# Kernel optimization log

Measured on AMD Instinct MI355X. Metric: run time of the kernel, lower is better.

Reference implementation:

```python
import jax, jax.numpy as jnp
import numpy as np

NHEAD = 16


def setup_inputs() -> dict:
    key = jax.random.key(0)
    ks = jax.random.split(key, 8)
    S, B, D = 2048, 2, 1024
    std = 1.0 / np.sqrt(D)
    src = jax.random.normal(ks[0], (S, B, D), dtype=jnp.float32)
    edge_bias_2d = jax.random.normal(ks[1], (S, S), dtype=jnp.float32)
    wq = jax.random.normal(ks[2], (D, D), dtype=jnp.float32) * std
    wk = jax.random.normal(ks[3], (D, D), dtype=jnp.float32) * std
    wv = jax.random.normal(ks[4], (D, D), dtype=jnp.float32) * std
    wo = jax.random.normal(ks[5], (D, D), dtype=jnp.float32) * std
    bq = jnp.zeros((D,), jnp.float32)
    bk = jnp.zeros((D,), jnp.float32)
    bv = jnp.zeros((D,), jnp.float32)
    bo = jnp.zeros((D,), jnp.float32)
    return {"src": src, "edge_bias_2d": edge_bias_2d, "wq": wq, "bq": bq,
            "wk": wk, "bk": bk, "wv": wv, "bv": bv, "wo": wo, "bo": bo}


def reference(src, edge_bias_2d, wq, bq, wk, bk, wv, bv, wo, bo):
    S, B, D = src.shape
    h = NHEAD
    hd = D // h
    scale = hd ** (-0.5)

    def heads(t):  # [S,B,D] -> [B,h,S,hd]
        return t.reshape(S, B, h, hd).transpose(1, 2, 0, 3)

    q = heads(src @ wq + bq)
    k = heads(src @ wk + bk)
    v = heads(src @ wv + bv)

    # [B,h,S,S]
    logits = jnp.einsum('bhsd,bhtd->bhst', q, k) * scale
    logits = logits + edge_bias_2d[None, None, :, :]
    attn = jax.nn.softmax(logits, axis=-1)
    # signed aggregation: sign(edge_bias) with 0 -> +1
    sign_gate = jnp.where(edge_bias_2d < 0, -1.0, 1.0).astype(attn.dtype)
    attn = attn * sign_gate[None, None, :, :]

    out = jnp.einsum('bhst,bhtd->bhsd', attn, v)  # [B,h,S,hd]
    out = out.transpose(2, 0, 1, 3).reshape(S, B, D)
    out = out @ wo + bo
    return out
```

## Files before the change

### kernel.cpp

```cpp
#include <hip/hip_runtime.h>
#include <stdint.h>

typedef unsigned short u16;
typedef unsigned int u32;

typedef __bf16 bf8 __attribute__((ext_vector_type(8)));
typedef bf8 bf8a __attribute__((may_alias));
typedef float f32x4 __attribute__((ext_vector_type(4)));
typedef uint2 uint2a __attribute__((may_alias));
typedef ushort4 ushort4a __attribute__((may_alias));
typedef float4 float4a __attribute__((may_alias));

#define MFMA_BF16(a, b, c) __builtin_amdgcn_mfma_f32_16x16x32_bf16((a), (b), (c), 0, 0, 0)

__device__ __forceinline__ u16 f2b(float x) {
  u32 u = __float_as_uint(x);
  return (u16)((u + 0x7fffu + ((u >> 16) & 1u)) >> 16);
}
__device__ __forceinline__ u32 pack2(float a, float b) {
  u32 ua = __float_as_uint(a), ub = __float_as_uint(b);
  return ((ua + 0x8000u) >> 16) | ((ub + 0x8000u) & 0xffff0000u);
}
__device__ __forceinline__ void async16(const u16* g, void* l) {
  __builtin_amdgcn_global_load_lds((const __attribute__((address_space(1))) u32*)g,
                                   (__attribute__((address_space(3))) u32*)l, 16, 0, 0);
}

__global__ __launch_bounds__(256) void convert_src(const float* __restrict__ src,
                                                   u16* __restrict__ dst) {
  const int i = blockIdx.x * 256 + threadIdx.x;
  float4 v = *(const float4a*)(src + i * 4);
  ushort4 o;
  o.x = f2b(v.x); o.y = f2b(v.y); o.z = f2b(v.z); o.w = f2b(v.w);
  *(ushort4a*)(dst + i * 4) = o;
}

__global__ __launch_bounds__(256) void prep_eb(const float* __restrict__ EB,
                                               u16* __restrict__ E2) {
  const int gid = blockIdx.x * 256 + threadIdx.x;
  const int s = gid >> 9;
  const int t = (gid & 511) * 4;
  const float4 v = *(const float4a*)(EB + s * 2048 + t);
  const float c2 = 1.44269504088896340736f;
  ushort4 o;
  o.x = f2b(__builtin_amdgcn_exp2f(v.x * c2)) | (u16)((__float_as_uint(v.x) >> 16) & 0x8000u);
  o.y = f2b(__builtin_amdgcn_exp2f(v.y * c2)) | (u16)((__float_as_uint(v.y) >> 16) & 0x8000u);
  o.z = f2b(__builtin_amdgcn_exp2f(v.z * c2)) | (u16)((__float_as_uint(v.z) >> 16) & 0x8000u);
  o.w = f2b(__builtin_amdgcn_exp2f(v.w * c2)) | (u16)((__float_as_uint(v.w) >> 16) & 0x8000u);
  const int ti = ((s >> 4) * 128 + (t >> 4)) * 256 + (s & 15) * 16 + (t & 15);
  *(ushort4a*)(E2 + ti) = o;
}

__global__ __launch_bounds__(256) void transpose4(
    const float* __restrict__ w0, const float* __restrict__ w1,
    const float* __restrict__ w2, const float* __restrict__ w3,
    u16* __restrict__ t0, u16* __restrict__ t1, u16* __restrict__ t2, u16* __restrict__ t3) {
  const int z = blockIdx.z;
  const float* W = z == 0 ? w0 : z == 1 ? w1 : z == 2 ? w2 : w3;
  u16* T = z == 0 ? t0 : z == 1 ? t1 : z == 2 ? t2 : t3;
  __shared__ __align__(8) u16 tile[64][68];
  const int tid = threadIdx.x;
  const int ty = tid >> 4, tx = tid & 15;
  const int kb = blockIdx.y * 64, nb = blockIdx.x * 64;
#pragma unroll
  for (int i = 0; i < 4; ++i) {
    int lk = ty + i * 16;
    float4 v = *(const float4a*)(W + (kb + lk) * 1024 + nb + tx * 4);
    ushort4 h;
    h.x = f2b(v.x); h.y = f2b(v.y); h.z = f2b(v.z); h.w = f2b(v.w);
    *(ushort4a*)&tile[lk][tx * 4] = h;
  }
  __syncthreads();
#pragma unroll
  for (int i = 0; i < 4; ++i) {
    int ln = ty + i * 16;
    ushort4 v;
    v.x = tile[tx * 4 + 0][ln];
    v.y = tile[tx * 4 + 1][ln];
    v.z = tile[tx * 4 + 2][ln];
    v.w = tile[tx * 4 + 3][ln];
    *(ushort4a*)(T + (nb + ln) * 1024 + kb + tx * 4) = v;
  }
}

__global__ __launch_bounds__(256) void gemm_bt(
    const u16* __restrict__ A,
    const u16* __restrict__ B0, const u16* __restrict__ B1, const u16* __restrict__ B2,
    const float* __restrict__ c0, const float* __restrict__ c1, const float* __restrict__ c2,
    u16* __restrict__ O0, u16* __restrict__ O1, u16* __restrict__ O2,
    float* __restrict__ Of, int plain) {
  __shared__ __align__(16) u16 sm[8192];
  u16* As = sm;
  u16* Bs = sm + 4096;
  const int tid = threadIdx.x, lane = tid & 63, w = tid >> 6;
  const int wm = w >> 1, wn = w & 1, quad = lane >> 4, l16 = lane & 15;
  const int z = blockIdx.z;
  const u16* Bt = z == 0 ? B0 : (z == 1 ? B1 : B2);
  const float* bi = z == 0 ? c0 : (z == 1 ? c1 : c2);
  u16* O = z == 0 ? O0 : (z == 1 ? O1 : O2);
  const int row0 = blockIdx.y * 128, col0 = blockIdx.x * 128;

  f32x4 acc[4][4];
#pragma unroll
  for (int i = 0; i < 4; ++i)
#pragma unroll
    for (int j = 0; j < 4; ++j) acc[i][j] = f32x4{0.f, 0.f, 0.f, 0.f};

  const int e0 = tid, e1 = tid + 256;
  const int r0 = e0 >> 2, cc0 = (e0 & 3) * 8;
  const int r1 = e1 >> 2, cc1 = (e1 & 3) * 8;
  const u32 lb0 = (u32)(w * 64) * 16;
  const u32 lb1 = (u32)(w * 64 + 256) * 16;

  for (int k0 = 0; k0 < 1024; k0 += 32) {
    __syncthreads();
    async16(A + (row0 + r0) * 1024 + k0 + cc0, (char*)As + lb0);
    async16(A + (row0 + r1) * 1024 + k0 + cc1, (char*)As + lb1);
    async16(Bt + (col0 + r0) * 1024 + k0 + cc0, (char*)Bs + lb0);
    async16(Bt + (col0 + r1) * 1024 + k0 + cc1, (char*)Bs + lb1);
    __syncthreads();
    bf8a af[4], bfr[4];
#pragma unroll
    for (int i = 0; i < 4; ++i) {
      af[i] = *(const bf8a*)(As + (wm * 64 + i * 16 + l16) * 32 + quad * 8);
      bfr[i] = *(const bf8a*)(Bs + (wn * 64 + i * 16 + l16) * 32 + quad * 8);
    }
#pragma unroll
    for (int mt = 0; mt < 4; ++mt)
#pragma unroll
      for (int nt = 0; nt < 4; ++nt) acc[mt][nt] = MFMA_BF16(af[mt], bfr[nt], acc[mt][nt]);
  }

#pragma unroll
  for (int nt = 0; nt < 4; ++nt) {
    const int col = col0 + wn * 64 + nt * 16 + l16;
    const float bcol = bi[col];
#pragma unroll
    for (int mt = 0; mt < 4; ++mt) {
#pragma unroll
      for (int r = 0; r < 4; ++r) {
        const int rm = row0 + wm * 64 + mt * 16 + quad * 4 + r;
        const float fv = acc[mt][nt][r] + bcol;
        if (plain) {
          Of[rm * 1024 + col] = fv;
        } else {
          const u16 hv = f2b(fv);
          const int s = rm >> 1, b_ = rm & 1, hh = col >> 6, e = col & 63;
          const int p = b_ * 16 + hh;
          if (z < 2) O[(p * 2048 + s) * 64 + e] = hv;
          else O[(p * 64 + e) * 2048 + s] = hv;
        }
      }
    }
  }
}

#define STAGE_K(Ksbuf, kt_)                                                         \
  {                                                                                 \
    _Pragma("unroll") for (int c = 0; c < 4; ++c) {                                 \
      const int row_ = c * 32 + w * 8 + r8;                                         \
      async16(Kp + ((kt_) * 128 + row_) * 64 + c16s * 8,                            \
              (char*)(Ksbuf) + (c * 4 + w) * 1024);                                 \
    }                                                                               \
  }

#define LOAD_E(eb, kt_)                                                             \
  {                                                                                 \
    const int tb16_ = (kt_) * 8 + w * 2;                                            \
    _Pragma("unroll") for (int st = 0; st < 4; ++st)                                \
      _Pragma("unroll") for (int tt = 0; tt < 2; ++tt)                              \
        eb[st][tt] = *(const uint2a*)(EBp + ((qt * 4 + st) * 128 + tb16_ + tt) * 256 \
                                      + l16 * 16 + quad * 4);                       \
  }

#define COMPUTE(Ksbuf, eb, kt_)                                                     \
  {                                                                                 \
    const int tb_ = (kt_) * 128 + w * 32;                                           \
    bf8a vf[4];            \
    _Pragma("unroll") for (int nt = 0; nt < 4; ++nt)                                \
      vf[nt] = *(const bf8a*)(Vp + (nt * 16 + l16) * 2048 + tb_ + quad * 8);        \
    bf8a kf[2][2];                                                                  \
    _Pragma("unroll") for (int tt = 0; tt < 2; ++tt) {                              \
      const int row_ = w * 32 + tt * 16 + l16;                 \
      _Pragma("unroll") for (int ks = 0; ks < 2; ++ks) {                            \
        const int cc_ = ((ks * 4 + quad) ^ (l16 & 7)) * 8;                          \
        kf[tt][ks] = *(const bf8a*)((Ksbuf) + row_ * 64 + cc_);                     \
      }                                                                             \
    }                                                                               \
    f32x4 sacc[4][2];                                                 \
    __builtin_amdgcn_s_setprio(1);                                                  \
    _Pragma("unroll") for (int tt = 0; tt < 2; ++tt)                                \
      _Pragma("unroll") for (int st = 0; st < 4; ++st) {                            \
        f32x4 t0_ = f32x4{0.f, 0.f, 0.f, 0.f};                                      \
        t0_ = MFMA_BF16(kf[tt][0], qf[st][0], t0_);                                 \
        sacc[st][tt] = MFMA_BF16(kf[tt][1], qf[st][1], t0_);                        \
      }                                                                             \
    __builtin_amdgcn_s_setprio(0);                                                  \
    _Pragma("unroll") for (int st = 0; st < 4; ++st) {                              \
      _Pragma("unroll") for (int tt = 0; tt < 2; ++tt) {                            \
        const uint2 e_ = eb[st][tt];                                                \
        const float g0 = __uint_as_float(e_.x << 16);                               \
        const float g1 = __uint_as_float(e_.x & 0xffff0000u);                       \
        const float g2 = __uint_as_float(e_.y << 16);                               \
        const float g3 = __uint_as_float(e_.y & 0xffff0000u);                       \
        const float p0 = __builtin_amdgcn_exp2f(sacc[st][tt][0] * c1) * g0;         \
        const float p1 = __builtin_amdgcn_exp2f(sacc[st][tt][1] * c1) * g1;         \
        const float p2 = __builtin_amdgcn_exp2f(sacc[st][tt][2] * c1) * g2;         \
        const float p3 = __builtin_amdgcn_exp2f(sacc[st][tt][3] * c1) * g3;         \
        lsum[st] += (__builtin_fabsf(p0) + __builtin_fabsf(p1)) +                   \
                    (__builtin_fabsf(p2) + __builtin_fabsf(p3));                    \
        uint2 v_;                                                                   \
        v_.x = pack2(p0, p1);                                                       \
        v_.y = pack2(p2, p3);                                                       \
        *(uint2a*)(Pw + st * 1152 + l16 * 72 + tt * 32 + quad * 8) = v_;            \
      }                                                                             \
    }                                                                               \
    _Pragma("unroll") for (int st = 0; st < 4; ++st) {                              \
      bf8a pf = *(const bf8a*)(Pw + st * 1152 + l16 * 72 + quad * 16);              \
      __builtin_amdgcn_s_setprio(1);                                                \
      _Pragma("unroll") for (int nt = 0; nt < 4; ++nt)                              \
        oacc[st][nt] = MFMA_BF16(vf[nt], pf, oacc[st][nt]);                         \
      __builtin_amdgcn_s_setprio(0);                                                \
    }                                                                               \
  }

__global__ __launch_bounds__(256, 2) void attn_fused(
    const u16* __restrict__ Qw, const u16* __restrict__ Kw, const u16* __restrict__ Vw,
    const u16* __restrict__ EBp, u16* __restrict__ Ao) {
  __shared__ __align__(16) char smem[51456];
  u16* const Ks0 = (u16*)smem;
  u16* const Ks1 = (u16*)(smem + 16384);
  const int tid = threadIdx.x, lane = tid & 63, w = tid >> 6;
  const int quad = lane >> 4, l16 = lane & 15;
  const int id = blockIdx.x;
  const int xcd = id & 7, idx = id >> 3;
  const int pair = xcd * 4 + (idx & 3);
  const int qt = idx >> 2;
  const int bb = pair >> 4, hh = pair & 15;
  const u16* Qp = Qw + pair * (2048 * 64);
  const u16* Kp = Kw + pair * (2048 * 64);
  const u16* Vp = Vw + pair * (64 * 2048);
  const int s0 = qt * 64;
  char* const Pw = smem + 32768 + w * 4608;

  bf8a qf[4][2];
#pragma unroll
  for (int st = 0; st < 4; ++st)
#pragma unroll
    for (int ks = 0; ks < 2; ++ks)
      qf[st][ks] = *(const bf8a*)(Qp + (s0 + st * 16 + l16) * 64 + ks * 32 + quad * 8);

  f32x4 oacc[4][4];
#pragma unroll
  for (int i = 0; i < 4; ++i)
#pragma unroll
    for (int j = 0; j < 4; ++j) oacc[i][j] = f32x4{0.f, 0.f, 0.f, 0.f};
  float lsum[4] = {0.f, 0.f, 0.f, 0.f};
  const float c1 = 0.125f * 1.44269504088896340736f;

  const int r8 = lane >> 3;
  const int c16s = (lane & 7) ^ r8;

  uint2 ebA[4][2], ebB[4][2];

  STAGE_K(Ks0, 0)
  LOAD_E(ebA, 0)
  __syncthreads();

  for (int kt = 0; kt < 16; kt += 2) {
    STAGE_K(Ks1, kt + 1)
    LOAD_E(ebB, kt + 1)
    COMPUTE(Ks0, ebA, kt)
    __syncthreads();
    if (kt < 14) {
      STAGE_K(Ks0, kt + 2)
      LOAD_E(ebA, kt + 2)
    }
    COMPUTE(Ks1, ebB, kt + 1)
    __syncthreads();
  }

  float* const Obuf = (float*)smem;
  float* const Lbuf = (float*)(smem + 51200);
#pragma unroll
  for (int st = 0; st < 4; ++st) {
    float ls = lsum[st];
    ls += __shfl_xor(ls, 16);
    ls += __shfl_xor(ls, 32);
    if (lane < 16) Lbuf[w * 16 + l16] = ls;
#pragma unroll
    for (int nt = 0; nt < 4; ++nt)
      *(float4a*)&Obuf[w * 1056 + l16 * 66 + nt * 16 + quad * 4] = (float4){
          oacc[st][nt][0], oacc[st][nt][1], oacc[st][nt][2], oacc[st][nt][3]};
    __syncthreads();
    {
      const int s_ = tid & 15, eg = (tid >> 4) * 4;
      float a0 = 0.f, a1 = 0.f, a2 = 0.f, a3 = 0.f;
#pragma unroll
      for (int wp = 0; wp < 4; ++wp) {
        const float4 x = *(const float4a*)&Obuf[wp * 1056 + s_ * 66 + eg];
        a0 += x.x; a1 += x.y; a2 += x.z; a3 += x.w;
      }
      const float lt = Lbuf[s_] + Lbuf[16 + s_] + Lbuf[32 + s_] + Lbuf[48 + s_];
      const float inv = 1.0f / lt;
      ushort4 o;
      o.x = f2b(a0 * inv); o.y = f2b(a1 * inv); o.z = f2b(a2 * inv); o.w = f2b(a3 * inv);
      *(ushort4a*)(Ao + ((s0 + st * 16 + s_) * 2 + bb) * 1024 + hh * 64 + eg) = o;
    }
    if (st < 3) __syncthreads();
  }
}

extern "C" void kernel_launch(void* const* d_in, const int* in_sizes, int n_in,
                              void* d_out, int out_size, void* d_ws, size_t ws_size,
                              hipStream_t stream) {
  const float* src = (const float*)d_in[0];
  const float* eb = (const float*)d_in[1];
  const float* wq = (const float*)d_in[2];
  const float* bq = (const float*)d_in[3];
  const float* wk = (const float*)d_in[4];
  const float* bk = (const float*)d_in[5];
  const float* wv = (const float*)d_in[6];
  const float* bv = (const float*)d_in[7];
  const float* wo = (const float*)d_in[8];
  const float* bo = (const float*)d_in[9];
  u16* ws = (u16*)d_ws;
  const size_t MM = 1024 * 1024;
  u16* wqT = ws;
  u16* wkT = ws + MM;
  u16* wvT = ws + 2 * MM;
  u16* woT = ws + 3 * MM;
  u16* srcB = ws + 4 * MM;
  u16* eb2 = ws + 4 * MM;
  u16* qW = ws + 8 * MM;
  u16* kW = ws + 12 * MM;
  u16* vW = ws + 16 * MM;
  u16* aO = ws + 20 * MM;
  float* out = (float*)d_out;

  convert_src<<<dim3(4096), 256, 0, stream>>>(src, srcB);
  transpose4<<<dim3(16, 16, 4), 256, 0, stream>>>(wq, wk, wv, wo, wqT, wkT, wvT, woT);
  gemm_bt<<<dim3(8, 32, 3), 256, 0, stream>>>(srcB, wqT, wkT, wvT, bq, bk, bv,
                                              qW, kW, vW, nullptr, 0);
  prep_eb<<<dim3(4096), 256, 0, stream>>>(eb, eb2);
  attn_fused<<<dim3(1024), 256, 0, stream>>>(qW, kW, vW, eb2, aO);
  gemm_bt<<<dim3(8, 32, 1), 256, 0, stream>>>(aO, woT, woT, woT, bo, bo, bo,
                                              nullptr, nullptr, nullptr, out, 1);
}
```

Before: 259.2 us.

## Fold softmax scale into Q projection, merge prep kernels, raise attention occupancy

Merges the source conversion and weight transpose into one launch. Folds the softmax scale and log2e factor into the Q projection epilogue so the attention kernel skips a multiply per score. Restructures the attention compute to process one 16-key sub-tile at a time, load the edge-bias tiles inside the compute step instead of double-buffering them in registers, and load V fragments later. Together these cut register pressure enough to request 3 blocks per SM instead of 2. It also switches P packing to the compiler's bf16 conversion. The cost is less latency hiding for the bias loads, and scaled Q is now rounded to bf16 after scaling, which slightly changes numerics.

```diff
diff --git a/kernel.cpp b/kernel.cpp
--- a/kernel.cpp
+++ b/kernel.cpp
@@ -17,22 +17,52 @@
   u32 u = __float_as_uint(x);
   return (u16)((u + 0x7fffu + ((u >> 16) & 1u)) >> 16);
 }
-__device__ __forceinline__ u32 pack2(float a, float b) {
-  u32 ua = __float_as_uint(a), ub = __float_as_uint(b);
-  return ((ua + 0x8000u) >> 16) | ((ub + 0x8000u) & 0xffff0000u);
-}
 __device__ __forceinline__ void async16(const u16* g, void* l) {
   __builtin_amdgcn_global_load_lds((const __attribute__((address_space(1))) u32*)g,
                                    (__attribute__((address_space(3))) u32*)l, 16, 0, 0);
 }
 
-__global__ __launch_bounds__(256) void convert_src(const float* __restrict__ src,
-                                                   u16* __restrict__ dst) {
-  const int i = blockIdx.x * 256 + threadIdx.x;
-  float4 v = *(const float4a*)(src + i * 4);
-  ushort4 o;
-  o.x = f2b(v.x); o.y = f2b(v.y); o.z = f2b(v.z); o.w = f2b(v.w);
-  *(ushort4a*)(dst + i * 4) = o;
+__global__ __launch_bounds__(256) void prep_inputs(
+    const float* __restrict__ src, u16* __restrict__ dst,
+    const float* __restrict__ w0, const float* __restrict__ w1,
+    const float* __restrict__ w2, const float* __restrict__ w3,
+    u16* __restrict__ t0, u16* __restrict__ t1, u16* __restrict__ t2, u16* __restrict__ t3) {
+  const int bid = blockIdx.x, tid = threadIdx.x;
+  if (bid < 4096) {
+    const int i = bid * 256 + tid;
+    float4 v = *(const float4a*)(src + i * 4);
+    ushort4 o;
+    o.x = f2b(v.x); o.y = f2b(v.y); o.z = f2b(v.z); o.w = f2b(v.w);
+    *(ushort4a*)(dst + i * 4) = o;
+    return;
+  }
+  const int b2 = bid - 4096;
+  const int z = b2 >> 8, xy = b2 & 255;
+  const int bx = xy & 15, by = xy >> 4;
+  const float* W = z == 0 ? w0 : z == 1 ? w1 : z == 2 ? w2 : w3;
+  u16* T = z == 0 ? t0 : z == 1 ? t1 : z == 2 ? t2 : t3;
+  __shared__ __align__(8) u16 tile[64][68];
+  const int ty = tid >> 4, tx = tid & 15;
+  const int kb = by * 64, nb = bx * 64;
+#pragma unroll
+  for (int i = 0; i < 4; ++i) {
+    int lk = ty + i * 16;
+    float4 v = *(const float4a*)(W + (kb + lk) * 1024 + nb + tx * 4);
+    ushort4 h;
+    h.x = f2b(v.x); h.y = f2b(v.y); h.z = f2b(v.z); h.w = f2b(v.w);
+    *(ushort4a*)&tile[lk][tx * 4] = h;
+  }
+  __syncthreads();
+#pragma unroll
+  for (int i = 0; i < 4; ++i) {
+    int ln = ty + i * 16;
+    ushort4 v;
+    v.x = tile[tx * 4 + 0][ln];
+    v.y = tile[tx * 4 + 1][ln];
+    v.z = tile[tx * 4 + 2][ln];
+    v.w = tile[tx * 4 + 3][ln];
+    *(ushort4a*)(T + (nb + ln) * 1024 + kb + tx * 4) = v;
+  }
 }
 
 __global__ __launch_bounds__(256) void prep_eb(const float* __restrict__ EB,
@@ -51,42 +81,11 @@
   *(ushort4a*)(E2 + ti) = o;
 }
 
-__global__ __launch_bounds__(256) void transpose4(
-    const float* __restrict__ w0, const float* __restrict__ w1,
-    const float* __restrict__ w2, const float* __restrict__ w3,
-    u16* __restrict__ t0, u16* __restrict__ t1, u16* __restrict__ t2, u16* __restrict__ t3) {
-  const int z = blockIdx.z;
-  const float* W = z == 0 ? w0 : z == 1 ? w1 : z == 2 ? w2 : w3;
-  u16* T = z == 0 ? t0 : z == 1 ? t1 : z == 2 ? t2 : t3;
-  __shared__ __align__(8) u16 tile[64][68];
-  const int tid = threadIdx.x;
-  const int ty = tid >> 4, tx = tid & 15;
-  const int kb = blockIdx.y * 64, nb = blockIdx.x * 64;
-#pragma unroll
-  for (int i = 0; i < 4; ++i) {
-    int lk = ty + i * 16;
-    float4 v = *(const float4a*)(W + (kb + lk) * 1024 + nb + tx * 4);
-    ushort4 h;
-    h.x = f2b(v.x); h.y = f2b(v.y); h.z = f2b(v.z); h.w = f2b(v.w);
-    *(ushort4a*)&tile[lk][tx * 4] = h;
-  }
-  __syncthreads();
-#pragma unroll
-  for (int i = 0; i < 4; ++i) {
-    int ln = ty + i * 16;
-    ushort4 v;
-    v.x = tile[tx * 4 + 0][ln];
-    v.y = tile[tx * 4 + 1][ln];
-    v.z = tile[tx * 4 + 2][ln];
-    v.w = tile[tx * 4 + 3][ln];
-    *(ushort4a*)(T + (nb + ln) * 1024 + kb + tx * 4) = v;
-  }
-}
-
 __global__ __launch_bounds__(256) void gemm_bt(
     const u16* __restrict__ A,
     const u16* __restrict__ B0, const u16* __restrict__ B1, const u16* __restrict__ B2,
     const float* __restrict__ c0, const float* __restrict__ c1, const float* __restrict__ c2,
+    float sc0, float sc1, float sc2,
     u16* __restrict__ O0, u16* __restrict__ O1, u16* __restrict__ O2,
     float* __restrict__ Of, int plain) {
   __shared__ __align__(16) u16 sm[8192];
@@ -97,6 +96,7 @@
   const int z = blockIdx.z;
   const u16* Bt = z == 0 ? B0 : (z == 1 ? B1 : B2);
   const float* bi = z == 0 ? c0 : (z == 1 ? c1 : c2);
+  const float sc = z == 0 ? sc0 : (z == 1 ? sc1 : sc2);
   u16* O = z == 0 ? O0 : (z == 1 ? O1 : O2);
   const int row0 = blockIdx.y * 128, col0 = blockIdx.x * 128;
 
@@ -140,7 +140,7 @@
 #pragma unroll
       for (int r = 0; r < 4; ++r) {
         const int rm = row0 + wm * 64 + mt * 16 + quad * 4 + r;
-        const float fv = acc[mt][nt][r] + bcol;
+        const float fv = (acc[mt][nt][r] + bcol) * sc;
         if (plain) {
           Of[rm * 1024 + col] = fv;
         } else {
@@ -164,57 +164,57 @@
     }                                                                               \
   }
 
-#define LOAD_E(eb, kt_)                                                             \
+#define COMPUTE(Ksbuf, kt_)                                                         \
   {                                                                                 \
     const int tb16_ = (kt_) * 8 + w * 2;                                            \
-    _Pragma("unroll") for (int st = 0; st < 4; ++st)                                \
-      _Pragma("unroll") for (int tt = 0; tt < 2; ++tt)                              \
-        eb[st][tt] = *(const uint2a*)(EBp + ((qt * 4 + st) * 128 + tb16_ + tt) * 256 \
-                                      + l16 * 16 + quad * 4);                       \
-  }
-
-#define COMPUTE(Ksbuf, eb, kt_)                                                     \
-  {                                                                                 \
-    const int tb_ = (kt_) * 128 + w * 32;                                           \
-    bf8a vf[4];            \
-    _Pragma("unroll") for (int nt = 0; nt < 4; ++nt)                                \
-      vf[nt] = *(const bf8a*)(Vp + (nt * 16 + l16) * 2048 + tb_ + quad * 8);        \
-    bf8a kf[2][2];                                                                  \
+    uint2 ebt[2][4];                          \
+    _Pragma("unroll") for (int tt = 0; tt < 2; ++tt)                                \
+      _Pragma("unroll") for (int st = 0; st < 4; ++st)                              \
+        ebt[tt][st] = *(const uint2a*)(EBp + ((qt * 4 + st) * 128 + tb16_ + tt) * 256 \
+                                       + l16 * 16 + quad * 4);                      \
     _Pragma("unroll") for (int tt = 0; tt < 2; ++tt) {                              \
-      const int row_ = w * 32 + tt * 16 + l16;                 \
-      _Pragma("unroll") for (int ks = 0; ks < 2; ++ks) {                            \
-        const int cc_ = ((ks * 4 + quad) ^ (l16 & 7)) * 8;                          \
-        kf[tt][ks] = *(const bf8a*)((Ksbuf) + row_ * 64 + cc_);                     \
+      bf8a kfa[2];                                                                  \
+      {                                                                             \
+        const int row_ = w * 32 + tt * 16 + l16;               \
+        _Pragma("unroll") for (int ks = 0; ks < 2; ++ks) {                          \
+          const int cc_ = ((ks * 4 + quad) ^ (l16 & 7)) * 8;                        \
+          kfa[ks] = *(const bf8a*)((Ksbuf) + row_ * 64 + cc_);                      \
+        }                                                                           \
       }                                                                             \
-    }                                                                               \
-    f32x4 sacc[4][2];                                                 \
-    __builtin_amdgcn_s_setprio(1);                                                  \
-    _Pragma("unroll") for (int tt = 0; tt < 2; ++tt)                                \
+      f32x4 sacc[4];                                                                \
+      __builtin_amdgcn_s_setprio(1);                                                \
       _Pragma("unroll") for (int st = 0; st < 4; ++st) {                            \
         f32x4 t0_ = f32x4{0.f, 0.f, 0.f, 0.f};                                      \
-        t0_ = MFMA_BF16(kf[tt][0], qf[st][0], t0_);                                 \
-        sacc[st][tt] = MFMA_BF16(kf[tt][1], qf[st][1], t0_);                        \
+        t0_ = MFMA_BF16(kfa[0], qf[st][0], t0_);                                    \
+        sacc[st] = MFMA_BF16(kfa[1], qf[st][1], t0_);                               \
       }                                                                             \
-    __builtin_amdgcn_s_setprio(0);                                                  \
-    _Pragma("unroll") for (int st = 0; st < 4; ++st) {                              \
-      _Pragma("unroll") for (int tt = 0; tt < 2; ++tt) {                            \
-        const uint2 e_ = eb[st][tt];                                                \
+      __builtin_amdgcn_s_setprio(0);                                                \
+      _Pragma("unroll") for (int st = 0; st < 4; ++st) {                            \
+        const uint2 e_ = ebt[tt][st];                                               \
         const float g0 = __uint_as_float(e_.x << 16);                               \
         const float g1 = __uint_as_float(e_.x & 0xffff0000u);                       \
         const float g2 = __uint_as_float(e_.y << 16);                               \
         const float g3 = __uint_as_float(e_.y & 0xffff0000u);                       \
-        const float p0 = __builtin_amdgcn_exp2f(sacc[st][tt][0] * c1) * g0;         \
-        const float p1 = __builtin_amdgcn_exp2f(sacc[st][tt][1] * c1) * g1;         \
-        const float p2 = __builtin_amdgcn_exp2f(sacc[st][tt][2] * c1) * g2;         \
-        const float p3 = __builtin_amdgcn_exp2f(sacc[st][tt][3] * c1) * g3;         \
+        const float p0 = __builtin_amdgcn_exp2f(sacc[st][0]) * g0;                  \
+        const float p1 = __builtin_amdgcn_exp2f(sacc[st][1]) * g1;                  \
+        const float p2 = __builtin_amdgcn_exp2f(sacc[st][2]) * g2;                  \
+        const float p3 = __builtin_amdgcn_exp2f(sacc[st][3]) * g3;                  \
         lsum[st] += (__builtin_fabsf(p0) + __builtin_fabsf(p1)) +                   \
                     (__builtin_fabsf(p2) + __builtin_fabsf(p3));                    \
+        const u16 h0 = __builtin_bit_cast(u16, (__bf16)p0);                         \
+        const u16 h1 = __builtin_bit_cast(u16, (__bf16)p1);                         \
+        const u16 h2 = __builtin_bit_cast(u16, (__bf16)p2);                         \
+        const u16 h3 = __builtin_bit_cast(u16, (__bf16)p3);                         \
         uint2 v_;                                                                   \
-        v_.x = pack2(p0, p1);                                                       \
-        v_.y = pack2(p2, p3);                                                       \
+        v_.x = (u32)h0 | ((u32)h1 << 16);                                           \
+        v_.y = (u32)h2 | ((u32)h3 << 16);                                           \
         *(uint2a*)(Pw + st * 1152 + l16 * 72 + tt * 32 + quad * 8) = v_;            \
       }                                                                             \
     }                                                                               \
+    const int tb_ = (kt_) * 128 + w * 32;                                           \
+    bf8a vf[4];              \
+    _Pragma("unroll") for (int nt = 0; nt < 4; ++nt)                                \
+      vf[nt] = *(const bf8a*)(Vp + (nt * 16 + l16) * 2048 + tb_ + quad * 8);        \
     _Pragma("unroll") for (int st = 0; st < 4; ++st) {                              \
       bf8a pf = *(const bf8a*)(Pw + st * 1152 + l16 * 72 + quad * 16);              \
       __builtin_amdgcn_s_setprio(1);                                                \
@@ -224,7 +224,7 @@
     }                                                                               \
   }
 
-__global__ __launch_bounds__(256, 2) void attn_fused(
+__global__ __launch_bounds__(256, 3) void attn_fused(
     const u16* __restrict__ Qw, const u16* __restrict__ Kw, const u16* __restrict__ Vw,
     const u16* __restrict__ EBp, u16* __restrict__ Ao) {
   __shared__ __align__(16) char smem[51456];
@@ -256,27 +256,21 @@
 #pragma unroll
     for (int j = 0; j < 4; ++j) oacc[i][j] = f32x4{0.f, 0.f, 0.f, 0.f};
   float lsum[4] = {0.f, 0.f, 0.f, 0.f};
-  const float c1 = 0.125f * 1.44269504088896340736f;
 
   const int r8 = lane >> 3;
   const int c16s = (lane & 7) ^ r8;
 
-  uint2 ebA[4][2], ebB[4][2];
-
   STAGE_K(Ks0, 0)
-  LOAD_E(ebA, 0)
   __syncthreads();
 
   for (int kt = 0; kt < 16; kt += 2) {
     STAGE_K(Ks1, kt + 1)
-    LOAD_E(ebB, kt + 1)
-    COMPUTE(Ks0, ebA, kt)
+    COMPUTE(Ks0, kt)
     __syncthreads();
     if (kt < 14) {
       STAGE_K(Ks0, kt + 2)
-      LOAD_E(ebA, kt + 2)
     }
-    COMPUTE(Ks1, ebB, kt + 1)
+    COMPUTE(Ks1, kt + 1)
     __syncthreads();
   }
 
@@ -337,13 +331,16 @@
   u16* vW = ws + 16 * MM;
   u16* aO = ws + 20 * MM;
   float* out = (float*)d_out;
-
-  convert_src<<<dim3(4096), 256, 0, stream>>>(src, srcB);
-  transpose4<<<dim3(16, 16, 4), 256, 0, stream>>>(wq, wk, wv, wo, wqT, wkT, wvT, woT);
+  const float c1 = 0.125f * 1.44269504088896340736f;
+
+  prep_inputs<<<dim3(5120), 256, 0, stream>>>(src, srcB, wq, wk, wv, wo,
+                                              wqT, wkT, wvT, woT);
   gemm_bt<<<dim3(8, 32, 3), 256, 0, stream>>>(srcB, wqT, wkT, wvT, bq, bk, bv,
+                                              c1, 1.0f, 1.0f,
                                               qW, kW, vW, nullptr, 0);
   prep_eb<<<dim3(4096), 256, 0, stream>>>(eb, eb2);
   attn_fused<<<dim3(1024), 256, 0, stream>>>(qW, kW, vW, eb2, aO);
   gemm_bt<<<dim3(8, 32, 1), 256, 0, stream>>>(aO, woT, woT, woT, bo, bo, bo,
+                                              1.0f, 1.0f, 1.0f,
                                               nullptr, nullptr, nullptr, out, 1);
 }
```

Result: slower. 331.8 us (+28.0%).
